# Optimization experiments

Hardware: AMD Instinct MI355X
Metric: run time of the kernel (lower is better)

Reference implementation:

```python
import jax, jax.numpy as jnp
import numpy as np

N, E, F, H, C, B, V, K = 50000, 800000, 256, 256, 10, 128, 4, 3
P_DROP, P_NODE, LAM = 0.5, 0.5, 1.0


def setup_inputs() -> dict:
    key = jax.random.key(0)
    ks = jax.random.split(key, 10)
    x = jax.random.normal(ks[0], (N, F), dtype=jnp.float32)
    edge_index = jax.random.randint(ks[1], (2, E), 0, N, dtype=jnp.int64)
    batch = jnp.sort(jax.random.randint(ks[2], (N,), 0, B, dtype=jnp.int64))
    # F.dropout mask (keep/(1-p) scaling) and drop_node masks (no rescale)
    dropout_mask = jax.random.bernoulli(ks[3], 1.0 - P_DROP, (N, F)).astype(jnp.float32) / (1.0 - P_DROP)
    node_masks = jax.random.bernoulli(ks[4], 1.0 - P_NODE, (V, N)).astype(jnp.float32)
    s1 = 1.0 / np.sqrt(F)
    s2 = 1.0 / np.sqrt(H)
    W1 = jax.random.normal(ks[5], (F, H), dtype=jnp.float32) * s1
    b1 = jnp.zeros((H,), dtype=jnp.float32)
    W2 = jax.random.normal(ks[6], (H, H), dtype=jnp.float32) * s2
    b2 = jnp.zeros((H,), dtype=jnp.float32)
    Wc = jax.random.normal(ks[7], (H, C), dtype=jnp.float32) * s2
    bc = jnp.zeros((C,), dtype=jnp.float32)
    return dict(x=x, edge_index=edge_index, batch=batch, dropout_mask=dropout_mask,
                node_masks=node_masks, W1=W1, b1=b1, W2=W2, b2=b2, Wc=Wc, bc=bc)


def reference(x, edge_index, batch, dropout_mask, node_masks, W1, b1, W2, b2, Wc, bc):
    # add self loops
    self_idx = jnp.arange(N, dtype=edge_index.dtype)
    row = jnp.concatenate([edge_index[0], self_idx])
    col = jnp.concatenate([edge_index[1], self_idx])
    deg = jax.ops.segment_sum(jnp.ones_like(row, dtype=jnp.float32), row, num_segments=N)
    norm = 1.0 / jnp.clip(deg, 1.0)[row]          # [E+N]

    counts = jnp.clip(jax.ops.segment_sum(jnp.ones((N,), jnp.float32), batch, num_segments=B), 1.0)

    x0 = x * dropout_mask                          # F.dropout (training)

    def per_view(mask):
        xv = x0 * mask[:, None]                    # drop_node
        for _ in range(K):                         # gather-scale-scatter_add
            xv = jax.ops.segment_sum(xv[col] * norm[:, None], row, num_segments=N)
        h = jax.nn.relu(xv @ W1 + b1) @ W2 + b2    # MLP
        gsum = jax.ops.segment_sum(h, batch, num_segments=B)
        return gsum / counts[:, None]              # global_mean_pool -> [B, H]

    views = jax.vmap(per_view)(node_masks)         # [V, B, H]

    logits = views[0] @ Wc + bc                    # [B, C]
    probs = jax.nn.softmax(jax.lax.stop_gradient(views) @ Wc + bc, axis=-1)  # [V, B, C]
    mean_probs = jnp.mean(probs, axis=0)           # [B, C]
    loss_cons = jnp.mean(jnp.sum((probs - mean_probs[None]) ** 2, axis=-1))
    loss_ent = -jnp.mean(jnp.sum(mean_probs * jnp.log(mean_probs + 1e-8), axis=-1))
    loss = LAM * loss_cons + loss_ent
    return logits, loss
```

## Files before the change

kernel.cpp:

```cpp
#include <hip/hip_runtime.h>
#include <hip/hip_bf16.h>
#include <hip/hip_fp16.h>

#define NN 50000
#define EE 800000
#define FF 256
#define HH 256
#define CC 10
#define BB 128
#define VV 4
#define SS 16
#define NBLK 196
#define NB64 782
#define NSLAB 16

typedef _Float16 half8v __attribute__((ext_vector_type(8)));
typedef float f32x4 __attribute__((ext_vector_type(4)));
typedef unsigned int uint4v __attribute__((ext_vector_type(4)));

__device__ inline float2 h2f(unsigned int u) {
  __half2 h = *reinterpret_cast<__half2*>(&u);
  return __half22float2(h);
}
__device__ inline void fp8x4_to_f32(unsigned int u, float* f) {
  auto lo = __builtin_amdgcn_cvt_pk_f32_fp8(u, false);
  auto hi = __builtin_amdgcn_cvt_pk_f32_fp8(u, true);
  f[0] = lo[0]; f[1] = lo[1]; f[2] = hi[0]; f[3] = hi[1];
}
__device__ inline unsigned int f32x4_to_fp8(float a, float b, float c, float d) {
  int u = __builtin_amdgcn_cvt_pk_fp8_f32(a, b, 0, false);
  u = __builtin_amdgcn_cvt_pk_fp8_f32(c, d, u, true);
  return (unsigned int)u;
}

__global__ __launch_bounds__(256) void k_deg(const int* __restrict__ row, int* __restrict__ deg) {
  int i = blockIdx.x * 256 + threadIdx.x;
  if (i < EE) atomicAdd(&deg[row[i]], 1);
}

__global__ __launch_bounds__(256) void k_scan1(const int* __restrict__ deg, int* __restrict__ bsum) {
  int i = blockIdx.x * 256 + threadIdx.x;
  int v = (i < NN) ? deg[i] : 0;
  for (int o = 32; o > 0; o >>= 1) v += __shfl_down(v, o, 64);
  __shared__ int ws[4];
  if ((threadIdx.x & 63) == 0) ws[threadIdx.x >> 6] = v;
  __syncthreads();
  if (threadIdx.x == 0) bsum[blockIdx.x] = ws[0] + ws[1] + ws[2] + ws[3];
}

__global__ __launch_bounds__(256) void k_scan2(const int* __restrict__ bsum, int* __restrict__ boff) {
  __shared__ int tmp[256];
  int tid = threadIdx.x;
  int v = (tid < NBLK) ? bsum[tid] : 0;
  tmp[tid] = v;
  __syncthreads();
  for (int o = 1; o < 256; o <<= 1) {
    int t = 0;
    if (tid >= o) t = tmp[tid - o];
    __syncthreads();
    if (tid >= o) tmp[tid] += t;
    __syncthreads();
  }
  if (tid < NBLK) boff[tid] = tmp[tid] - v;
}

__global__ __launch_bounds__(256) void k_scan3(const int* __restrict__ deg,
                                               const int* __restrict__ boff,
                                               int* __restrict__ rptr) {
  __shared__ int tmp[256];
  int tid = threadIdx.x;
  int i = blockIdx.x * 256 + tid;
  int v = (i < NN) ? deg[i] : 0;
  tmp[tid] = v;
  __syncthreads();
  for (int o = 1; o < 256; o <<= 1) {
    int t = 0;
    if (tid >= o) t = tmp[tid - o];
    __syncthreads();
    if (tid >= o) tmp[tid] += t;
    __syncthreads();
  }
  int incl = tmp[tid];
  if (i < NN) rptr[i] = boff[blockIdx.x] + incl - v;
  if (i == NN - 1) rptr[NN] = boff[blockIdx.x] + incl;
}

__global__ __launch_bounds__(256) void k_scatter(const int* __restrict__ row,
                                                 const int* __restrict__ col,
                                                 const int* __restrict__ rptr,
                                                 int* __restrict__ fill,
                                                 int* __restrict__ csort) {
  int i = blockIdx.x * 256 + threadIdx.x;
  if (i < EE) {
    int r = row[i];
    int p = rptr[r] + atomicAdd(&fill[r], 1);
    csort[p] = col[i];
  }
}

__global__ __launch_bounds__(256) void k_bptr(const int* __restrict__ batch, int* __restrict__ bptr) {
  int b = threadIdx.x;
  if (b > BB) return;
  int lo = 0, hi = NN;
  while (lo < hi) { int mid = (lo + hi) >> 1; if (batch[mid] < b) lo = mid + 1; else hi = mid; }
  bptr[b] = lo;
}

__global__ __launch_bounds__(256) void k_packm(const float* __restrict__ nmask, float4* __restrict__ m4) {
  int i = blockIdx.x * 256 + threadIdx.x;
  if (i < NN)
    m4[i] = make_float4(nmask[i], nmask[NN + i], nmask[2 * NN + i], nmask[3 * NN + i]);
}

__global__ __launch_bounds__(256) void k_wfrag(const float* __restrict__ W, _Float16* __restrict__ wf) {
  int id = blockIdx.x * 256 + threadIdx.x;
  if (id >= 8 * 16 * 64) return;
  int lane = id & 63;
  int t = (id >> 6) & 15;
  int ks = id >> 10;
  int n = t * 16 + (lane & 15);
  int k0 = ks * 32 + (lane >> 4) * 8;
  half8v v;
#pragma unroll
  for (int j = 0; j < 8; ++j) v[j] = (_Float16)W[(size_t)(k0 + j) * HH + n];
  reinterpret_cast<half8v*>(wf)[id] = v;
}

__global__ __launch_bounds__(256) void k_gemm(const float* __restrict__ X,
                                              const float* __restrict__ DM,
                                              const _Float16* __restrict__ wf,
                                              __half* __restrict__ Z) {
  int w = threadIdx.x >> 6, lane = threadIdx.x & 63;
  int arow = blockIdx.x * 64 + w * 16 + (lane & 15);
  bool valid = arow < NN;
  const half8v* wfv = reinterpret_cast<const half8v*>(wf);
  f32x4 acc[16];
#pragma unroll
  for (int t = 0; t < 16; ++t) acc[t] = (f32x4){0.f, 0.f, 0.f, 0.f};
  for (int ks = 0; ks < 8; ++ks) {
    int k0 = ks * 32 + (lane >> 4) * 8;
    half8v a;
    if (valid) {
      const float4* xp = reinterpret_cast<const float4*>(X + (size_t)arow * FF + k0);
      const float4* dp = reinterpret_cast<const float4*>(DM + (size_t)arow * FF + k0);
      float4 x0 = xp[0], x1 = xp[1], d0 = dp[0], d1 = dp[1];
      a[0] = (_Float16)(x0.x * d0.x); a[1] = (_Float16)(x0.y * d0.y);
      a[2] = (_Float16)(x0.z * d0.z); a[3] = (_Float16)(x0.w * d0.w);
      a[4] = (_Float16)(x1.x * d1.x); a[5] = (_Float16)(x1.y * d1.y);
      a[6] = (_Float16)(x1.z * d1.z); a[7] = (_Float16)(x1.w * d1.w);
    } else {
#pragma unroll
      for (int j = 0; j < 8; ++j) a[j] = (_Float16)0.f;
    }
#pragma unroll
    for (int t = 0; t < 16; ++t) {
      half8v b = wfv[(size_t)(ks * 16 + t) * 64 + lane];
      acc[t] = __builtin_amdgcn_mfma_f32_16x16x32_f16(a, b, acc[t], 0, 0, 0);
    }
  }
  int mrow = blockIdx.x * 64 + w * 16 + (lane >> 4) * 4;
  int ncol = lane & 15;
#pragma unroll
  for (int t = 0; t < 16; ++t) {
#pragma unroll
    for (int r = 0; r < 4; ++r) {
      int rr = mrow + r;
      if (rr < NN) Z[(size_t)rr * HH + t * 16 + ncol] = __float2half(acc[t][r]);
    }
  }
}

__global__ __launch_bounds__(256) void k_cvt8s(const __half* __restrict__ y,
                                               unsigned int* __restrict__ y8s) {
  int i = blockIdx.x * 256 + threadIdx.x;
  if (i >= NN * 64) return;
  int n = i >> 6;
  int sq = i & 63;
  int s = sq >> 2, q = sq & 3;
  const uint2* yp = reinterpret_cast<const uint2*>(y + (size_t)n * FF + s * 16 + q * 4);
  uint2 raw = *yp;
  float2 lo = h2f(raw.x), hi = h2f(raw.y);
  y8s[((size_t)s * NN + n) * 4 + q] = f32x4_to_fp8(lo.x, lo.y, hi.x, hi.y);
}

__device__ inline void slab_decode(int b, int& slab, int& nb) {
  int xcd = b & 7;
  int j = b >> 3;
  int half = (j >= NB64) ? 1 : 0;
  slab = xcd + 8 * half;
  nb = j - half * NB64;
}

__global__ __launch_bounds__(256) void k_prop1s(const unsigned int* __restrict__ y8s,
                                                uint4v* __restrict__ h8,
                                                const int* __restrict__ rptr,
                                                const int* __restrict__ csort,
                                                const float4* __restrict__ m4) {
  int slab, nb;
  slab_decode(blockIdx.x, slab, nb);
  int t4 = threadIdx.x & 3;
  int node = nb * 64 + (threadIdx.x >> 2);
  if (node >= NN) return;
  const unsigned int* ip = y8s + (size_t)slab * NN * 4;
  int s = rptr[node], e = rptr[node + 1];
  float acc[16];
  {
    float f[4];
    fp8x4_to_f32(ip[(size_t)node * 4 + t4], f);
    float4 m = m4[node];
#pragma unroll
    for (int k = 0; k < 4; ++k) {
      acc[k] = f[k] * m.x; acc[4 + k] = f[k] * m.y;
      acc[8 + k] = f[k] * m.z; acc[12 + k] = f[k] * m.w;
    }
  }
  int j = s;
  for (; j + 1 < e; j += 2) {
    int c0 = csort[j], c1 = csort[j + 1];
    float f0[4], f1[4];
    fp8x4_to_f32(ip[(size_t)c0 * 4 + t4], f0);
    fp8x4_to_f32(ip[(size_t)c1 * 4 + t4], f1);
    float4 p = m4[c0], q = m4[c1];
#pragma unroll
    for (int k = 0; k < 4; ++k) {
      acc[k]      += f0[k] * p.x + f1[k] * q.x;
      acc[4 + k]  += f0[k] * p.y + f1[k] * q.y;
      acc[8 + k]  += f0[k] * p.z + f1[k] * q.z;
      acc[12 + k] += f0[k] * p.w + f1[k] * q.w;
    }
  }
  if (j < e) {
    int c0 = csort[j];
    float f0[4];
    fp8x4_to_f32(ip[(size_t)c0 * 4 + t4], f0);
    float4 p = m4[c0];
#pragma unroll
    for (int k = 0; k < 4; ++k) {
      acc[k] += f0[k] * p.x; acc[4 + k] += f0[k] * p.y;
      acc[8 + k] += f0[k] * p.z; acc[12 + k] += f0[k] * p.w;
    }
  }
  float sc = 1.0f / (float)(e - s + 1);
  uint4v o;
  o.x = f32x4_to_fp8(acc[0] * sc, acc[1] * sc, acc[2] * sc, acc[3] * sc);
  o.y = f32x4_to_fp8(acc[4] * sc, acc[5] * sc, acc[6] * sc, acc[7] * sc);
  o.z = f32x4_to_fp8(acc[8] * sc, acc[9] * sc, acc[10] * sc, acc[11] * sc);
  o.w = f32x4_to_fp8(acc[12] * sc, acc[13] * sc, acc[14] * sc, acc[15] * sc);
  __builtin_nontemporal_store(o, &h8[((size_t)slab * NN + node) * 4 + t4]);
}

__global__ __launch_bounds__(256) void k_prop2s(const uint4v* __restrict__ in,
                                                uint4v* __restrict__ out,
                                                const int* __restrict__ rptr,
                                                const int* __restrict__ csort) {
  int slab, nb;
  slab_decode(blockIdx.x, slab, nb);
  int t4 = threadIdx.x & 3;
  int node = nb * 64 + (threadIdx.x >> 2);
  if (node >= NN) return;
  const uint4v* ip = in + (size_t)slab * NN * 4;
  int s = rptr[node], e = rptr[node + 1];
  float acc[16];
  {
    uint4v r = ip[(size_t)node * 4 + t4];
    fp8x4_to_f32(r.x, acc); fp8x4_to_f32(r.y, acc + 4);
    fp8x4_to_f32(r.z, acc + 8); fp8x4_to_f32(r.w, acc + 12);
  }
  int j = s;
  for (; j + 1 < e; j += 2) {
    int c0 = csort[j], c1 = csort[j + 1];
    uint4v r0 = ip[(size_t)c0 * 4 + t4];
    uint4v r1 = ip[(size_t)c1 * 4 + t4];
    float f0[16], f1[16];
    fp8x4_to_f32(r0.x, f0); fp8x4_to_f32(r0.y, f0 + 4);
    fp8x4_to_f32(r0.z, f0 + 8); fp8x4_to_f32(r0.w, f0 + 12);
    fp8x4_to_f32(r1.x, f1); fp8x4_to_f32(r1.y, f1 + 4);
    fp8x4_to_f32(r1.z, f1 + 8); fp8x4_to_f32(r1.w, f1 + 12);
#pragma unroll
    for (int k = 0; k < 16; ++k) acc[k] += f0[k] + f1[k];
  }
  if (j < e) {
    int c0 = csort[j];
    uint4v r0 = ip[(size_t)c0 * 4 + t4];
    float f0[16];
    fp8x4_to_f32(r0.x, f0); fp8x4_to_f32(r0.y, f0 + 4);
    fp8x4_to_f32(r0.z, f0 + 8); fp8x4_to_f32(r0.w, f0 + 12);
#pragma unroll
    for (int k = 0; k < 16; ++k) acc[k] += f0[k];
  }
  float sc = 1.0f / (float)(e - s + 1);
  uint4v o;
  o.x = f32x4_to_fp8(acc[0] * sc, acc[1] * sc, acc[2] * sc, acc[3] * sc);
  o.y = f32x4_to_fp8(acc[4] * sc, acc[5] * sc, acc[6] * sc, acc[7] * sc);
  o.z = f32x4_to_fp8(acc[8] * sc, acc[9] * sc, acc[10] * sc, acc[11] * sc);
  o.w = f32x4_to_fp8(acc[12] * sc, acc[13] * sc, acc[14] * sc, acc[15] * sc);
  __builtin_nontemporal_store(o, &out[((size_t)slab * NN + node) * 4 + t4]);
}

__global__ __launch_bounds__(256) void k_prop3s(const uint4v* __restrict__ in,
                                                const int* __restrict__ rptr,
                                                const int* __restrict__ csort,
                                                const int* __restrict__ batch,
                                                const float* __restrict__ b1,
                                                float* __restrict__ part) {
  int slab, nb;
  slab_decode(blockIdx.x, slab, nb);
  int tid = threadIdx.x;
  int t4 = tid & 3;
  int lane = tid & 63;
  int wid = tid >> 6;
  int node = nb * 64 + (tid >> 2);
  bool valid = node < NN;
  int nclamp = valid ? node : NN - 1;
  __shared__ float red[4][64];
  __shared__ int sbuni, sbatch;
  {
    int first = nb * 64;
    int last = first + 63; if (last >= NN) last = NN - 1;
    if (tid == 0) { sbatch = batch[first]; sbuni = (batch[first] == batch[last]); }
  }
  __syncthreads();
  const uint4v* ip = in + (size_t)slab * NN * 4;
  float acc[16];
#pragma unroll
  for (int k = 0; k < 16; ++k) acc[k] = 0.f;
  if (valid) {
    int s = rptr[node], e = rptr[node + 1];
    {
      uint4v r = ip[(size_t)node * 4 + t4];
      fp8x4_to_f32(r.x, acc); fp8x4_to_f32(r.y, acc + 4);
      fp8x4_to_f32(r.z, acc + 8); fp8x4_to_f32(r.w, acc + 12);
    }
    int j = s;
    for (; j + 1 < e; j += 2) {
      int c0 = csort[j], c1 = csort[j + 1];
      uint4v r0 = ip[(size_t)c0 * 4 + t4];
      uint4v r1 = ip[(size_t)c1 * 4 + t4];
      float f0[16], f1[16];
      fp8x4_to_f32(r0.x, f0); fp8x4_to_f32(r0.y, f0 + 4);
      fp8x4_to_f32(r0.z, f0 + 8); fp8x4_to_f32(r0.w, f0 + 12);
      fp8x4_to_f32(r1.x, f1); fp8x4_to_f32(r1.y, f1 + 4);
      fp8x4_to_f32(r1.z, f1 + 8); fp8x4_to_f32(r1.w, f1 + 12);
#pragma unroll
      for (int k = 0; k < 16; ++k) acc[k] += f0[k] + f1[k];
    }
    if (j < e) {
      int c0 = csort[j];
      uint4v r0 = ip[(size_t)c0 * 4 + t4];
      float f0[16];
      fp8x4_to_f32(r0.x, f0); fp8x4_to_f32(r0.y, f0 + 4);
      fp8x4_to_f32(r0.z, f0 + 8); fp8x4_to_f32(r0.w, f0 + 12);
#pragma unroll
      for (int k = 0; k < 16; ++k) acc[k] += f0[k];
    }
    float sc = 1.0f / (float)(e - s + 1);
    float4 bv = *reinterpret_cast<const float4*>(&b1[slab * 16 + t4 * 4]);
    float bk[4] = {bv.x, bv.y, bv.z, bv.w};
#pragma unroll
    for (int v = 0; v < 4; ++v)
#pragma unroll
      for (int k = 0; k < 4; ++k)
        acc[v * 4 + k] = fmaxf(acc[v * 4 + k] * sc + bk[k], 0.f);
  }
  int strip = nb & (SS - 1);
  int bn = batch[nclamp];
  if (sbuni) {
#pragma unroll
    for (int k = 0; k < 16; ++k) {
      acc[k] += __shfl_xor(acc[k], 4, 64);
      acc[k] += __shfl_xor(acc[k], 8, 64);
      acc[k] += __shfl_xor(acc[k], 16, 64);
      acc[k] += __shfl_xor(acc[k], 32, 64);
    }
    if (lane < 4) {
#pragma unroll
      for (int k = 0; k < 16; ++k) red[wid][lane * 16 + k] = acc[k];
    }
    __syncthreads();
    if (tid < 64) {
      float sum = red[0][tid] + red[1][tid] + red[2][tid] + red[3][tid];
      int l4 = tid >> 4, k = tid & 15;
      int view = k >> 2, fk = k & 3;
      int feat = slab * 16 + l4 * 4 + fk;
      atomicAdd(&part[(((size_t)view * SS + strip) * BB + sbatch) * HH + feat], sum);
    }
  } else {
    int bn0 = __shfl(bn, 0, 64);
    bool wuni = __all(bn == bn0);
    if (wuni) {
#pragma unroll
      for (int k = 0; k < 16; ++k) {
        acc[k] += __shfl_xor(acc[k], 4, 64);
        acc[k] += __shfl_xor(acc[k], 8, 64);
        acc[k] += __shfl_xor(acc[k], 16, 64);
        acc[k] += __shfl_xor(acc[k], 32, 64);
      }
      if (lane < 4) {
#pragma unroll
        for (int k = 0; k < 16; ++k) {
          int view = k >> 2, fk = k & 3;
          int feat = slab * 16 + lane * 4 + fk;
          atomicAdd(&part[(((size_t)view * SS + strip) * BB + bn0) * HH + feat], acc[k]);
        }
      }
    } else if (valid) {
#pragma unroll
      for (int k = 0; k < 16; ++k) {
        int view = k >> 2, fk = k & 3;
        int feat = slab * 16 + t4 * 4 + fk;
        atomicAdd(&part[(((size_t)view * SS + strip) * BB + bn) * HH + feat], acc[k]);
      }
    }
  }
}

__global__ __launch_bounds__(256) void k_head(const float* __restrict__ part,
                                              const int* __restrict__ bptr,
                                              const float* __restrict__ W2,
                                              const float* __restrict__ b2,
                                              const float* __restrict__ Wc,
                                              const float* __restrict__ bc,
                                              float* __restrict__ probs,
                                              float* __restrict__ logits) {
  int v = blockIdx.x / BB;
  int b = blockIdx.x % BB;
  int h = threadIdx.x;
  __shared__ float mr[HH];
  __shared__ float vr[HH];
  __shared__ float scs[CC];
  float acc = 0.f;
  for (int s = 0; s < SS; ++s)
    acc += part[(((size_t)v * SS + s) * BB + b) * HH + h];
  int cnt = bptr[b + 1] - bptr[b]; if (cnt < 1) cnt = 1;
  mr[h] = acc / (float)cnt;
  __syncthreads();
  float a = b2[h];
  for (int k = 0; k < HH; ++k) a += mr[k] * W2[k * HH + h];
  vr[h] = a;
  __syncthreads();
  if (h < CC) {
    float t = bc[h];
    for (int k = 0; k < HH; ++k) t += vr[k] * Wc[k * CC + h];
    scs[h] = t;
  }
  __syncthreads();
  if (h < CC) {
    float m = scs[0];
    for (int c = 1; c < CC; ++c) m = fmaxf(m, scs[c]);
    float den = 0.f;
    for (int c = 0; c < CC; ++c) den += expf(scs[c] - m);
    float p = expf(scs[h] - m) / den;
    probs[((size_t)v * BB + b) * CC + h] = p;
    if (v == 0) logits[b * CC + h] = scs[h];
  }
}

__global__ __launch_bounds__(256) void k_loss(const float* __restrict__ probs, float* __restrict__ out) {
  __shared__ float mp[BB * CC];
  __shared__ float red[8];
  int tid = threadIdx.x;
  float ent = 0.f;
  for (int i = tid; i < BB * CC; i += 256) {
    float m = 0.25f * (probs[i] + probs[BB * CC + i] + probs[2 * BB * CC + i] + probs[3 * BB * CC + i]);
    mp[i] = m;
    ent += m * logf(m + 1e-8f);
  }
  __syncthreads();
  float cons = 0.f;
  for (int i = tid; i < VV * BB * CC; i += 256) {
    float d = probs[i] - mp[i % (BB * CC)];
    cons += d * d;
  }
  for (int o = 32; o > 0; o >>= 1) {
    cons += __shfl_down(cons, o, 64);
    ent += __shfl_down(ent, o, 64);
  }
  int wid = tid >> 6, lane = tid & 63;
  if (lane == 0) { red[wid] = cons; red[4 + wid] = ent; }
  __syncthreads();
  if (tid == 0) {
    float c = red[0] + red[1] + red[2] + red[3];
    float e2 = red[4] + red[5] + red[6] + red[7];
    out[0] = c / (float)(VV * BB) - e2 / (float)BB;
  }
}

extern "C" void kernel_launch(void* const* d_in, const int* in_sizes, int n_in,
                              void* d_out, int out_size, void* d_ws, size_t ws_size,
                              hipStream_t stream) {
  const float* x     = (const float*)d_in[0];
  const int*   erow  = (const int*)d_in[1];
  const int*   ecol  = ((const int*)d_in[1]) + EE;
  const int*   batch = (const int*)d_in[2];
  const float* dm    = (const float*)d_in[3];
  const float* nmask = (const float*)d_in[4];
  const float* W1    = (const float*)d_in[5];
  const float* b1    = (const float*)d_in[6];
  const float* W2    = (const float*)d_in[7];
  const float* b2    = (const float*)d_in[8];
  const float* Wc    = (const float*)d_in[9];
  const float* bc    = (const float*)d_in[10];
  float* out = (float*)d_out;

  char* ws = (char*)d_ws;
  size_t off = 0;
  auto carve = [&](size_t bytes) -> char* {
    char* p = ws + off;
    off = (off + bytes + 255) & ~(size_t)255;
    return p;
  };
  float* part  = (float*)carve((size_t)VV * SS * BB * HH * 4);
  int*   deg   = (int*)carve((size_t)NN * 4);
  int*   fill  = (int*)carve((size_t)NN * 4);
  int*   rptr  = (int*)carve((size_t)(NN + 1) * 4);
  int*   csort = (int*)carve((size_t)EE * 4);
  int*   bptr  = (int*)carve((size_t)(BB + 1) * 4);
  int*   bsum  = (int*)carve(256 * 4);
  int*   boff  = (int*)carve(256 * 4);
  float* probs = (float*)carve((size_t)VV * BB * CC * 4);
  float4* m4   = (float4*)carve((size_t)NN * 16);
  _Float16* wf = (_Float16*)carve((size_t)8 * 16 * 64 * 8 * 2);

  const size_t NFh = (size_t)NN * FF * 2;
  __half* y  = (__half*)carve(NFh);
  unsigned int* y8s = (unsigned int*)carve((size_t)NN * 256);
  uint4v* h8a = (uint4v*)carve((size_t)NSLAB * NN * 64);
  uint4v* h8b = (uint4v*)carve((size_t)NSLAB * NN * 64);

  hipMemsetAsync(deg, 0, (size_t)NN * 4, stream);
  hipMemsetAsync(fill, 0, (size_t)NN * 4, stream);
  hipMemsetAsync(part, 0, (size_t)VV * SS * BB * HH * 4, stream);

  k_deg<<<(EE + 255) / 256, 256, 0, stream>>>(erow, deg);
  k_scan1<<<NBLK, 256, 0, stream>>>(deg, bsum);
  k_scan2<<<1, 256, 0, stream>>>(bsum, boff);
  k_scan3<<<NBLK, 256, 0, stream>>>(deg, boff, rptr);
  k_scatter<<<(EE + 255) / 256, 256, 0, stream>>>(erow, ecol, rptr, fill, csort);
  k_bptr<<<1, 256, 0, stream>>>(batch, bptr);
  k_packm<<<(NN + 255) / 256, 256, 0, stream>>>(nmask, m4);
  k_wfrag<<<32, 256, 0, stream>>>(W1, wf);

  k_gemm<<<(NN + 63) / 64, 256, 0, stream>>>(x, dm, wf, y);
  k_cvt8s<<<(NN * 64 + 255) / 256, 256, 0, stream>>>(y, y8s);
  k_prop1s<<<NSLAB * NB64, 256, 0, stream>>>(y8s, h8a, rptr, csort, m4);
  k_prop2s<<<NSLAB * NB64, 256, 0, stream>>>(h8a, h8b, rptr, csort);
  k_prop3s<<<NSLAB * NB64, 256, 0, stream>>>(h8b, rptr, csort, batch, b1, part);
  k_head<<<VV * BB, 256, 0, stream>>>(part, bptr, W2, b2, Wc, bc, probs, out);
  k_loss<<<1, 256, 0, stream>>>(probs, out + BB * CC);
}
```

Before: 691.2 us.

## Parallelize propagation over edges: one wavefront per node with shuffle reduction

New measurement: 1.936 ms. 2.8x slower.

```diff
diff --git a/kernel.cpp b/kernel.cpp
--- a/kernel.cpp
+++ b/kernel.cpp
@@ -11,8 +11,8 @@
 #define VV 4
 #define SS 16
 #define NBLK 196
-#define NB64 782
 #define NSLAB 16
+#define BPS 12500
 
 typedef _Float16 half8v __attribute__((ext_vector_type(8)));
 typedef float f32x4 __attribute__((ext_vector_type(4)));
@@ -186,27 +186,29 @@
 __device__ inline void slab_decode(int b, int& slab, int& nb) {
   int xcd = b & 7;
   int j = b >> 3;
-  int half = (j >= NB64) ? 1 : 0;
+  int half = (j >= BPS) ? 1 : 0;
   slab = xcd + 8 * half;
-  nb = j - half * NB64;
-}
-
-__global__ __launch_bounds__(256) void k_prop1s(const unsigned int* __restrict__ y8s,
+  nb = j - half * BPS;
+}
+
+__global__ __launch_bounds__(256) void k_prop1e(const unsigned int* __restrict__ y8s,
                                                 uint4v* __restrict__ h8,
                                                 const int* __restrict__ rptr,
                                                 const int* __restrict__ csort,
                                                 const float4* __restrict__ m4) {
   int slab, nb;
   slab_decode(blockIdx.x, slab, nb);
-  int t4 = threadIdx.x & 3;
-  int node = nb * 64 + (threadIdx.x >> 2);
-  if (node >= NN) return;
+  int w = threadIdx.x >> 6, lane = threadIdx.x & 63;
+  int g = lane >> 2, q = lane & 3;
+  int node = nb * 4 + w;
   const unsigned int* ip = y8s + (size_t)slab * NN * 4;
   int s = rptr[node], e = rptr[node + 1];
   float acc[16];
-  {
+#pragma unroll
+  for (int k = 0; k < 16; ++k) acc[k] = 0.f;
+  if (g == 0) {
     float f[4];
-    fp8x4_to_f32(ip[(size_t)node * 4 + t4], f);
+    fp8x4_to_f32(ip[(size_t)node * 4 + q], f);
     float4 m = m4[node];
 #pragma unroll
     for (int k = 0; k < 4; ++k) {
@@ -214,90 +216,82 @@
       acc[8 + k] = f[k] * m.z; acc[12 + k] = f[k] * m.w;
     }
   }
-  int j = s;
-  for (; j + 1 < e; j += 2) {
-    int c0 = csort[j], c1 = csort[j + 1];
-    float f0[4], f1[4];
-    fp8x4_to_f32(ip[(size_t)c0 * 4 + t4], f0);
-    fp8x4_to_f32(ip[(size_t)c1 * 4 + t4], f1);
-    float4 p = m4[c0], q = m4[c1];
+  for (int j = s + g; j < e; j += 16) {
+    int c = __builtin_nontemporal_load(&csort[j]);
+    float f[4];
+    fp8x4_to_f32(ip[(size_t)c * 4 + q], f);
+    float4 m = m4[c];
 #pragma unroll
     for (int k = 0; k < 4; ++k) {
-      acc[k]      += f0[k] * p.x + f1[k] * q.x;
-      acc[4 + k]  += f0[k] * p.y + f1[k] * q.y;
-      acc[8 + k]  += f0[k] * p.z + f1[k] * q.z;
-      acc[12 + k] += f0[k] * p.w + f1[k] * q.w;
-    }
-  }
-  if (j < e) {
-    int c0 = csort[j];
-    float f0[4];
-    fp8x4_to_f32(ip[(size_t)c0 * 4 + t4], f0);
-    float4 p = m4[c0];
-#pragma unroll
-    for (int k = 0; k < 4; ++k) {
-      acc[k] += f0[k] * p.x; acc[4 + k] += f0[k] * p.y;
-      acc[8 + k] += f0[k] * p.z; acc[12 + k] += f0[k] * p.w;
-    }
-  }
-  float sc = 1.0f / (float)(e - s + 1);
-  uint4v o;
-  o.x = f32x4_to_fp8(acc[0] * sc, acc[1] * sc, acc[2] * sc, acc[3] * sc);
-  o.y = f32x4_to_fp8(acc[4] * sc, acc[5] * sc, acc[6] * sc, acc[7] * sc);
-  o.z = f32x4_to_fp8(acc[8] * sc, acc[9] * sc, acc[10] * sc, acc[11] * sc);
-  o.w = f32x4_to_fp8(acc[12] * sc, acc[13] * sc, acc[14] * sc, acc[15] * sc);
-  __builtin_nontemporal_store(o, &h8[((size_t)slab * NN + node) * 4 + t4]);
-}
-
-__global__ __launch_bounds__(256) void k_prop2s(const uint4v* __restrict__ in,
+      acc[k] += f[k] * m.x; acc[4 + k] += f[k] * m.y;
+      acc[8 + k] += f[k] * m.z; acc[12 + k] += f[k] * m.w;
+    }
+  }
+#pragma unroll
+  for (int k = 0; k < 16; ++k) {
+    acc[k] += __shfl_xor(acc[k], 4, 64);
+    acc[k] += __shfl_xor(acc[k], 8, 64);
+    acc[k] += __shfl_xor(acc[k], 16, 64);
+    acc[k] += __shfl_xor(acc[k], 32, 64);
+  }
+  if (g == 0) {
+    float sc = 1.0f / (float)(e - s + 1);
+    uint4v o;
+    o.x = f32x4_to_fp8(acc[0] * sc, acc[1] * sc, acc[2] * sc, acc[3] * sc);
+    o.y = f32x4_to_fp8(acc[4] * sc, acc[5] * sc, acc[6] * sc, acc[7] * sc);
+    o.z = f32x4_to_fp8(acc[8] * sc, acc[9] * sc, acc[10] * sc, acc[11] * sc);
+    o.w = f32x4_to_fp8(acc[12] * sc, acc[13] * sc, acc[14] * sc, acc[15] * sc);
+    __builtin_nontemporal_store(o, &h8[((size_t)slab * NN + node) * 4 + q]);
+  }
+}
+
+__global__ __launch_bounds__(256) void k_prop2e(const uint4v* __restrict__ in,
                                                 uint4v* __restrict__ out,
                                                 const int* __restrict__ rptr,
                                                 const int* __restrict__ csort) {
   int slab, nb;
   slab_decode(blockIdx.x, slab, nb);
-  int t4 = threadIdx.x & 3;
-  int node = nb * 64 + (threadIdx.x >> 2);
-  if (node >= NN) return;
+  int w = threadIdx.x >> 6, lane = threadIdx.x & 63;
+  int g = lane >> 2, q = lane & 3;
+  int node = nb * 4 + w;
   const uint4v* ip = in + (size_t)slab * NN * 4;
   int s = rptr[node], e = rptr[node + 1];
   float acc[16];
-  {
-    uint4v r = ip[(size_t)node * 4 + t4];
+#pragma unroll
+  for (int k = 0; k < 16; ++k) acc[k] = 0.f;
+  if (g == 0) {
+    uint4v r = ip[(size_t)node * 4 + q];
     fp8x4_to_f32(r.x, acc); fp8x4_to_f32(r.y, acc + 4);
     fp8x4_to_f32(r.z, acc + 8); fp8x4_to_f32(r.w, acc + 12);
   }
-  int j = s;
-  for (; j + 1 < e; j += 2) {
-    int c0 = csort[j], c1 = csort[j + 1];
-    uint4v r0 = ip[(size_t)c0 * 4 + t4];
-    uint4v r1 = ip[(size_t)c1 * 4 + t4];
-    float f0[16], f1[16];
-    fp8x4_to_f32(r0.x, f0); fp8x4_to_f32(r0.y, f0 + 4);
-    fp8x4_to_f32(r0.z, f0 + 8); fp8x4_to_f32(r0.w, f0 + 12);
-    fp8x4_to_f32(r1.x, f1); fp8x4_to_f32(r1.y, f1 + 4);
-    fp8x4_to_f32(r1.z, f1 + 8); fp8x4_to_f32(r1.w, f1 + 12);
-#pragma unroll
-    for (int k = 0; k < 16; ++k) acc[k] += f0[k] + f1[k];
-  }
-  if (j < e) {
-    int c0 = csort[j];
-    uint4v r0 = ip[(size_t)c0 * 4 + t4];
-    float f0[16];
-    fp8x4_to_f32(r0.x, f0); fp8x4_to_f32(r0.y, f0 + 4);
-    fp8x4_to_f32(r0.z, f0 + 8); fp8x4_to_f32(r0.w, f0 + 12);
-#pragma unroll
-    for (int k = 0; k < 16; ++k) acc[k] += f0[k];
-  }
-  float sc = 1.0f / (float)(e - s + 1);
-  uint4v o;
-  o.x = f32x4_to_fp8(acc[0] * sc, acc[1] * sc, acc[2] * sc, acc[3] * sc);
-  o.y = f32x4_to_fp8(acc[4] * sc, acc[5] * sc, acc[6] * sc, acc[7] * sc);
-  o.z = f32x4_to_fp8(acc[8] * sc, acc[9] * sc, acc[10] * sc, acc[11] * sc);
-  o.w = f32x4_to_fp8(acc[12] * sc, acc[13] * sc, acc[14] * sc, acc[15] * sc);
-  __builtin_nontemporal_store(o, &out[((size_t)slab * NN + node) * 4 + t4]);
-}
-
-__global__ __launch_bounds__(256) void k_prop3s(const uint4v* __restrict__ in,
+  for (int j = s + g; j < e; j += 16) {
+    int c = __builtin_nontemporal_load(&csort[j]);
+    uint4v r = ip[(size_t)c * 4 + q];
+    float f[16];
+    fp8x4_to_f32(r.x, f); fp8x4_to_f32(r.y, f + 4);
+    fp8x4_to_f32(r.z, f + 8); fp8x4_to_f32(r.w, f + 12);
+#pragma unroll
+    for (int k = 0; k < 16; ++k) acc[k] += f[k];
+  }
+#pragma unroll
+  for (int k = 0; k < 16; ++k) {
+    acc[k] += __shfl_xor(acc[k], 4, 64);
+    acc[k] += __shfl_xor(acc[k], 8, 64);
+    acc[k] += __shfl_xor(acc[k], 16, 64);
+    acc[k] += __shfl_xor(acc[k], 32, 64);
+  }
+  if (g == 0) {
+    float sc = 1.0f / (float)(e - s + 1);
+    uint4v o;
+    o.x = f32x4_to_fp8(acc[0] * sc, acc[1] * sc, acc[2] * sc, acc[3] * sc);
+    o.y = f32x4_to_fp8(acc[4] * sc, acc[5] * sc, acc[6] * sc, acc[7] * sc);
+    o.z = f32x4_to_fp8(acc[8] * sc, acc[9] * sc, acc[10] * sc, acc[11] * sc);
+    o.w = f32x4_to_fp8(acc[12] * sc, acc[13] * sc, acc[14] * sc, acc[15] * sc);
+    __builtin_nontemporal_store(o, &out[((size_t)slab * NN + node) * 4 + q]);
+  }
+}
+
+__global__ __launch_bounds__(256) void k_prop3e(const uint4v* __restrict__ in,
                                                 const int* __restrict__ rptr,
                                                 const int* __restrict__ csort,
                                                 const int* __restrict__ batch,
@@ -306,110 +300,71 @@
   int slab, nb;
   slab_decode(blockIdx.x, slab, nb);
   int tid = threadIdx.x;
-  int t4 = tid & 3;
-  int lane = tid & 63;
-  int wid = tid >> 6;
-  int node = nb * 64 + (tid >> 2);
-  bool valid = node < NN;
-  int nclamp = valid ? node : NN - 1;
+  int w = tid >> 6, lane = tid & 63;
+  int g = lane >> 2, q = lane & 3;
+  int node = nb * 4 + w;
   __shared__ float red[4][64];
-  __shared__ int sbuni, sbatch;
-  {
-    int first = nb * 64;
-    int last = first + 63; if (last >= NN) last = NN - 1;
-    if (tid == 0) { sbatch = batch[first]; sbuni = (batch[first] == batch[last]); }
-  }
-  __syncthreads();
+  __shared__ int blkuni, b0s;
   const uint4v* ip = in + (size_t)slab * NN * 4;
+  int s = rptr[node], e = rptr[node + 1];
   float acc[16];
 #pragma unroll
   for (int k = 0; k < 16; ++k) acc[k] = 0.f;
-  if (valid) {
-    int s = rptr[node], e = rptr[node + 1];
-    {
-      uint4v r = ip[(size_t)node * 4 + t4];
-      fp8x4_to_f32(r.x, acc); fp8x4_to_f32(r.y, acc + 4);
-      fp8x4_to_f32(r.z, acc + 8); fp8x4_to_f32(r.w, acc + 12);
-    }
-    int j = s;
-    for (; j + 1 < e; j += 2) {
-      int c0 = csort[j], c1 = csort[j + 1];
-      uint4v r0 = ip[(size_t)c0 * 4 + t4];
-      uint4v r1 = ip[(size_t)c1 * 4 + t4];
-      float f0[16], f1[16];
-      fp8x4_to_f32(r0.x, f0); fp8x4_to_f32(r0.y, f0 + 4);
-      fp8x4_to_f32(r0.z, f0 + 8); fp8x4_to_f32(r0.w, f0 + 12);
-      fp8x4_to_f32(r1.x, f1); fp8x4_to_f32(r1.y, f1 + 4);
-      fp8x4_to_f32(r1.z, f1 + 8); fp8x4_to_f32(r1.w, f1 + 12);
-#pragma unroll
-      for (int k = 0; k < 16; ++k) acc[k] += f0[k] + f1[k];
-    }
-    if (j < e) {
-      int c0 = csort[j];
-      uint4v r0 = ip[(size_t)c0 * 4 + t4];
-      float f0[16];
-      fp8x4_to_f32(r0.x, f0); fp8x4_to_f32(r0.y, f0 + 4);
-      fp8x4_to_f32(r0.z, f0 + 8); fp8x4_to_f32(r0.w, f0 + 12);
-#pragma unroll
-      for (int k = 0; k < 16; ++k) acc[k] += f0[k];
-    }
+  if (g == 0) {
+    uint4v r = ip[(size_t)node * 4 + q];
+    fp8x4_to_f32(r.x, acc); fp8x4_to_f32(r.y, acc + 4);
+    fp8x4_to_f32(r.z, acc + 8); fp8x4_to_f32(r.w, acc + 12);
+  }
+  for (int j = s + g; j < e; j += 16) {
+    int c = __builtin_nontemporal_load(&csort[j]);
+    uint4v r = ip[(size_t)c * 4 + q];
+    float f[16];
+    fp8x4_to_f32(r.x, f); fp8x4_to_f32(r.y, f + 4);
+    fp8x4_to_f32(r.z, f + 8); fp8x4_to_f32(r.w, f + 12);
+#pragma unroll
+    for (int k = 0; k < 16; ++k) acc[k] += f[k];
+  }
+#pragma unroll
+  for (int k = 0; k < 16; ++k) {
+    acc[k] += __shfl_xor(acc[k], 4, 64);
+    acc[k] += __shfl_xor(acc[k], 8, 64);
+    acc[k] += __shfl_xor(acc[k], 16, 64);
+    acc[k] += __shfl_xor(acc[k], 32, 64);
+  }
+  float r16[16];
+  if (g == 0) {
     float sc = 1.0f / (float)(e - s + 1);
-    float4 bv = *reinterpret_cast<const float4*>(&b1[slab * 16 + t4 * 4]);
+    float4 bv = *reinterpret_cast<const float4*>(&b1[slab * 16 + q * 4]);
     float bk[4] = {bv.x, bv.y, bv.z, bv.w};
 #pragma unroll
     for (int v = 0; v < 4; ++v)
 #pragma unroll
       for (int k = 0; k < 4; ++k)
-        acc[v * 4 + k] = fmaxf(acc[v * 4 + k] * sc + bk[k], 0.f);
-  }
+        r16[v * 4 + k] = fmaxf(acc[v * 4 + k] * sc + bk[k], 0.f);
+#pragma unroll
+    for (int k = 0; k < 16; ++k) red[w][q * 16 + k] = r16[k];
+  }
+  if (tid == 0) {
+    b0s = batch[nb * 4];
+    blkuni = (batch[nb * 4] == batch[nb * 4 + 3]) ? 1 : 0;
+  }
+  __syncthreads();
   int strip = nb & (SS - 1);
-  int bn = batch[nclamp];
-  if (sbuni) {
-#pragma unroll
-    for (int k = 0; k < 16; ++k) {
-      acc[k] += __shfl_xor(acc[k], 4, 64);
-      acc[k] += __shfl_xor(acc[k], 8, 64);
-      acc[k] += __shfl_xor(acc[k], 16, 64);
-      acc[k] += __shfl_xor(acc[k], 32, 64);
-    }
-    if (lane < 4) {
-#pragma unroll
-      for (int k = 0; k < 16; ++k) red[wid][lane * 16 + k] = acc[k];
-    }
-    __syncthreads();
+  if (blkuni) {
     if (tid < 64) {
       float sum = red[0][tid] + red[1][tid] + red[2][tid] + red[3][tid];
-      int l4 = tid >> 4, k = tid & 15;
-      int view = k >> 2, fk = k & 3;
-      int feat = slab * 16 + l4 * 4 + fk;
-      atomicAdd(&part[(((size_t)view * SS + strip) * BB + sbatch) * HH + feat], sum);
-    }
-  } else {
-    int bn0 = __shfl(bn, 0, 64);
-    bool wuni = __all(bn == bn0);
-    if (wuni) {
-#pragma unroll
-      for (int k = 0; k < 16; ++k) {
-        acc[k] += __shfl_xor(acc[k], 4, 64);
-        acc[k] += __shfl_xor(acc[k], 8, 64);
-        acc[k] += __shfl_xor(acc[k], 16, 64);
-        acc[k] += __shfl_xor(acc[k], 32, 64);
-      }
-      if (lane < 4) {
-#pragma unroll
-        for (int k = 0; k < 16; ++k) {
-          int view = k >> 2, fk = k & 3;
-          int feat = slab * 16 + lane * 4 + fk;
-          atomicAdd(&part[(((size_t)view * SS + strip) * BB + bn0) * HH + feat], acc[k]);
-        }
-      }
-    } else if (valid) {
-#pragma unroll
-      for (int k = 0; k < 16; ++k) {
-        int view = k >> 2, fk = k & 3;
-        int feat = slab * 16 + t4 * 4 + fk;
-        atomicAdd(&part[(((size_t)view * SS + strip) * BB + bn) * HH + feat], acc[k]);
-      }
+      int qq = tid >> 4, idx = tid & 15;
+      int view = idx >> 2, k = idx & 3;
+      int feat = slab * 16 + qq * 4 + k;
+      atomicAdd(&part[(((size_t)view * SS + strip) * BB + b0s) * HH + feat], sum);
+    }
+  } else if (g == 0) {
+    int bn = batch[node];
+#pragma unroll
+    for (int k = 0; k < 16; ++k) {
+      int view = k >> 2, kk = k & 3;
+      int feat = slab * 16 + q * 4 + kk;
+      atomicAdd(&part[(((size_t)view * SS + strip) * BB + bn) * HH + feat], r16[k]);
     }
   }
 }
@@ -542,9 +497,9 @@
 
   k_gemm<<<(NN + 63) / 64, 256, 0, stream>>>(x, dm, wf, y);
   k_cvt8s<<<(NN * 64 + 255) / 256, 256, 0, stream>>>(y, y8s);
-  k_prop1s<<<NSLAB * NB64, 256, 0, stream>>>(y8s, h8a, rptr, csort, m4);
-  k_prop2s<<<NSLAB * NB64, 256, 0, stream>>>(h8a, h8b, rptr, csort);
-  k_prop3s<<<NSLAB * NB64, 256, 0, stream>>>(h8b, rptr, csort, batch, b1, part);
+  k_prop1e<<<NSLAB * BPS, 256, 0, stream>>>(y8s, h8a, rptr, csort, m4);
+  k_prop2e<<<NSLAB * BPS, 256, 0, stream>>>(h8a, h8b, rptr, csort);
+  k_prop3e<<<NSLAB * BPS, 256, 0, stream>>>(h8b, rptr, csort, batch, b1, part);
   k_head<<<VV * BB, 256, 0, stream>>>(part, bptr, W2, b2, Wc, bc, probs, out);
   k_loss<<<1, 256, 0, stream>>>(probs, out + BB * CC);
 }
```
